# Performance work log

Measured on AMD Instinct MI355X. Metric: run time of the kernel, lower is better.

Reference implementation:

```python
import jax, jax.numpy as jnp
import numpy as np

B, S, D = 8, 4096, 2048
E, TOP_K = 64, 2


def setup_inputs() -> dict:
    key = jax.random.key(0)
    kx, kw, kb = jax.random.split(key, 3)
    x = jax.random.normal(kx, (B, S, D), dtype=jnp.float32)
    # nn.Linear(input_dim, num_experts): weight [E, D], bias [E]
    bound = 1.0 / np.sqrt(D)
    W = jax.random.uniform(kw, (E, D), dtype=jnp.float32, minval=-bound, maxval=bound)
    b = jax.random.uniform(kb, (E,), dtype=jnp.float32, minval=-bound, maxval=bound)
    return {"x": x, "W": W, "b": b}


def reference(x, W, b):
    # mean-pool over sequence dim (x is 3D -> x.mean(dim=1))
    x_flat = jnp.mean(x, axis=1)                      # [B, D]
    logits = jnp.einsum('bd,ed->be', x_flat, W) + b   # [B, E]
    top_k_logits, top_k_indices = jax.lax.top_k(logits, TOP_K)  # [B, K] each
    weights = jax.nn.softmax(top_k_logits, axis=1)    # [B, K]
    return weights, top_k_indices
```

## Files before the change

### kernel.cpp

```cpp
#include <hip/hip_runtime.h>
#include <hip/hip_bf16.h>
#include <math.h>

#define BB 8
#define SS 4096
#define DD 2048
#define EE 64
#define NCHUNK 64
#define ROWS_PER_CHUNK (SS / NCHUNK)

__global__ void mean_partial_kernel(const float* __restrict__ x,
                                    float* __restrict__ partial) {
    int blk   = blockIdx.x;
    int h     = blk & 1;
    int c     = (blk >> 1) & (NCHUNK - 1);
    int b     = blk >> 7;
    int d     = h * (DD / 2) + threadIdx.x * 4;

    const float4* xp = (const float4*)(x + (size_t)b * SS * DD
                                         + (size_t)c * ROWS_PER_CHUNK * DD
                                         + d);
    float4 a0 = make_float4(0.f, 0.f, 0.f, 0.f);
    float4 a1 = make_float4(0.f, 0.f, 0.f, 0.f);
    float4 a2 = make_float4(0.f, 0.f, 0.f, 0.f);
    float4 a3 = make_float4(0.f, 0.f, 0.f, 0.f);
    const size_t rs = DD / 4;
    #pragma unroll 4
    for (int r = 0; r < ROWS_PER_CHUNK; r += 4) {
        float4 v0 = xp[(size_t)(r + 0) * rs];
        float4 v1 = xp[(size_t)(r + 1) * rs];
        float4 v2 = xp[(size_t)(r + 2) * rs];
        float4 v3 = xp[(size_t)(r + 3) * rs];
        a0.x += v0.x; a0.y += v0.y; a0.z += v0.z; a0.w += v0.w;
        a1.x += v1.x; a1.y += v1.y; a1.z += v1.z; a1.w += v1.w;
        a2.x += v2.x; a2.y += v2.y; a2.z += v2.z; a2.w += v2.w;
        a3.x += v3.x; a3.y += v3.y; a3.z += v3.z; a3.w += v3.w;
    }
    float4 acc;
    acc.x = (a0.x + a1.x) + (a2.x + a3.x);
    acc.y = (a0.y + a1.y) + (a2.y + a3.y);
    acc.z = (a0.z + a1.z) + (a2.z + a3.z);
    acc.w = (a0.w + a1.w) + (a2.w + a3.w);
    float4* pp = (float4*)(partial + ((size_t)c * BB + b) * DD + d);
    *pp = acc;
}

__global__ void gate_kernel(const float* __restrict__ partial,
                            const float* __restrict__ W,
                            const float* __restrict__ bias,
                            float* __restrict__ out) {
    __shared__ float xs[DD];
    __shared__ float lred[4][EE];
    __shared__ float logits[EE];

    int b   = blockIdx.x;
    int tid = threadIdx.x;

    for (int d = tid; d < DD; d += 256) {
        float s = 0.f;
        #pragma unroll 8
        for (int c = 0; c < NCHUNK; ++c)
            s += partial[((size_t)c * BB + b) * DD + d];
        xs[d] = s * (1.0f / SS);
    }
    __syncthreads();

    int e = tid & 63;
    int q = tid >> 6;
    const int QD = DD / 4;
    const float* wp = W + (size_t)e * DD + q * QD;
    const float* xq = xs + q * QD;
    float acc = 0.f;
    #pragma unroll 4
    for (int d = 0; d < QD; ++d) acc += xq[d] * wp[d];
    lred[q][e] = acc;
    __syncthreads();

    if (tid < EE) {
        logits[tid] = lred[0][tid] + lred[1][tid] + lred[2][tid] + lred[3][tid]
                      + bias[tid];
    }
    __syncthreads();

    if (tid == 0) {
        float m1 = -INFINITY, m2 = -INFINITY;
        int i1 = 0, i2 = 0;
        for (int i = 0; i < EE; ++i) {
            float v = logits[i];
            if (v > m1) { m2 = m1; i2 = i1; m1 = v; i1 = i; }
            else if (v > m2) { m2 = v; i2 = i; }
        }
        float e2 = expf(m2 - m1);
        float inv = 1.0f / (1.0f + e2);
        out[b * 2 + 0] = inv;
        out[b * 2 + 1] = e2 * inv;
        out[2 * BB + b * 2 + 0] = (float)i1;
        out[2 * BB + b * 2 + 1] = (float)i2;
    }
}

extern "C" void kernel_launch(void* const* d_in, const int* in_sizes, int n_in,
                              void* d_out, int out_size, void* d_ws, size_t ws_size,
                              hipStream_t stream) {
    const float* x  = (const float*)d_in[0];
    const float* W  = (const float*)d_in[1];
    const float* bb = (const float*)d_in[2];
    float* out      = (float*)d_out;
    float* partial  = (float*)d_ws;

    mean_partial_kernel<<<BB * NCHUNK * 2, 256, 0, stream>>>(x, partial);
    gate_kernel<<<BB, 256, 0, stream>>>(partial, W, bb, out);
}
```

Measured before the change: 401.8 us.

## Fuse gating dot product into streaming mean kernel, emit partial logits

The chunked sequence sum is now dotted with the matching half of W inside the streaming kernel using shared memory. Each block writes 64 partial logits instead of a 1024-float partial sum. The gate kernel then only reduces 128 partial logit vectors per batch, applies the 1/S scale and bias, and does top-2. This removes the slow serial reduction and dot product that ran in just 8 blocks. The cost is repeated W reads across blocks, which are expected to be served from cache, and more work per streaming block.

```diff
diff --git a/kernel.cpp b/kernel.cpp
--- a/kernel.cpp
+++ b/kernel.cpp
@@ -7,26 +7,32 @@
 #define DD 2048
 #define EE 64
 #define NCHUNK 64
-#define ROWS_PER_CHUNK (SS / NCHUNK)
+#define ROWS (SS / NCHUNK)
+#define NSLICE (NCHUNK * 2)
 
-__global__ void mean_partial_kernel(const float* __restrict__ x,
-                                    float* __restrict__ partial) {
-    int blk   = blockIdx.x;
-    int h     = blk & 1;
-    int c     = (blk >> 1) & (NCHUNK - 1);
-    int b     = blk >> 7;
-    int d     = h * (DD / 2) + threadIdx.x * 4;
+__global__ void __launch_bounds__(256, 4)
+fused_stream_kernel(const float* __restrict__ x,
+                    const float* __restrict__ W,
+                    float* __restrict__ plogit) {
+    __shared__ float xs[DD / 2];
+    __shared__ float lred[4][EE];
+
+    int blk = blockIdx.x;
+    int h   = blk & 1;
+    int c   = (blk >> 1) & (NCHUNK - 1);
+    int b   = blk >> 7;
+    int tid = threadIdx.x;
+    int d   = h * (DD / 2) + tid * 4;
 
     const float4* xp = (const float4*)(x + (size_t)b * SS * DD
-                                         + (size_t)c * ROWS_PER_CHUNK * DD
-                                         + d);
+                                         + (size_t)c * ROWS * DD + d);
     float4 a0 = make_float4(0.f, 0.f, 0.f, 0.f);
     float4 a1 = make_float4(0.f, 0.f, 0.f, 0.f);
     float4 a2 = make_float4(0.f, 0.f, 0.f, 0.f);
     float4 a3 = make_float4(0.f, 0.f, 0.f, 0.f);
     const size_t rs = DD / 4;
     #pragma unroll 4
-    for (int r = 0; r < ROWS_PER_CHUNK; r += 4) {
+    for (int r = 0; r < ROWS; r += 4) {
         float4 v0 = xp[(size_t)(r + 0) * rs];
         float4 v1 = xp[(size_t)(r + 1) * rs];
         float4 v2 = xp[(size_t)(r + 2) * rs];
@@ -41,44 +47,52 @@
     acc.y = (a0.y + a1.y) + (a2.y + a3.y);
     acc.z = (a0.z + a1.z) + (a2.z + a3.z);
     acc.w = (a0.w + a1.w) + (a2.w + a3.w);
-    float4* pp = (float4*)(partial + ((size_t)c * BB + b) * DD + d);
-    *pp = acc;
+    ((float4*)xs)[tid] = acc;
+    __syncthreads();
+
+    int e = tid & 63;
+    int q = tid >> 6;
+    const int QF4 = (DD / 2 / 4) / 4;
+    const float4* wp = (const float4*)(W + (size_t)e * DD
+                                         + h * (DD / 2) + q * (QF4 * 4));
+    const float4* xq = (const float4*)(xs + q * (QF4 * 4));
+    float dot = 0.f;
+    #pragma unroll 8
+    for (int i = 0; i < QF4; ++i) {
+        float4 wv = wp[i];
+        float4 xv = xq[i];
+        dot += wv.x * xv.x + wv.y * xv.y + wv.z * xv.z + wv.w * xv.w;
+    }
+    lred[q][e] = dot;
+    __syncthreads();
+
+    if (tid < EE) {
+        plogit[(size_t)blk * EE + tid] =
+            lred[0][tid] + lred[1][tid] + lred[2][tid] + lred[3][tid];
+    }
 }
 
-__global__ void gate_kernel(const float* __restrict__ partial,
-                            const float* __restrict__ W,
+__global__ void gate_kernel(const float* __restrict__ plogit,
                             const float* __restrict__ bias,
                             float* __restrict__ out) {
-    __shared__ float xs[DD];
     __shared__ float lred[4][EE];
     __shared__ float logits[EE];
 
     int b   = blockIdx.x;
     int tid = threadIdx.x;
+    int e   = tid & 63;
+    int g   = tid >> 6;
 
-    for (int d = tid; d < DD; d += 256) {
-        float s = 0.f;
-        #pragma unroll 8
-        for (int c = 0; c < NCHUNK; ++c)
-            s += partial[((size_t)c * BB + b) * DD + d];
-        xs[d] = s * (1.0f / SS);
-    }
-    __syncthreads();
-
-    int e = tid & 63;
-    int q = tid >> 6;
-    const int QD = DD / 4;
-    const float* wp = W + (size_t)e * DD + q * QD;
-    const float* xq = xs + q * QD;
-    float acc = 0.f;
-    #pragma unroll 4
-    for (int d = 0; d < QD; ++d) acc += xq[d] * wp[d];
-    lred[q][e] = acc;
+    float s = 0.f;
+    #pragma unroll 8
+    for (int j = g * (NSLICE / 4); j < (g + 1) * (NSLICE / 4); ++j)
+        s += plogit[((size_t)b * NSLICE + j) * EE + e];
+    lred[g][e] = s;
     __syncthreads();
 
     if (tid < EE) {
-        logits[tid] = lred[0][tid] + lred[1][tid] + lred[2][tid] + lred[3][tid]
-                      + bias[tid];
+        logits[tid] = (lred[0][tid] + lred[1][tid] + lred[2][tid] + lred[3][tid])
+                      * (1.0f / SS) + bias[tid];
     }
     __syncthreads();
 
@@ -106,8 +120,8 @@
     const float* W  = (const float*)d_in[1];
     const float* bb = (const float*)d_in[2];
     float* out      = (float*)d_out;
-    float* partial  = (float*)d_ws;
+    float* plogit   = (float*)d_ws;
 
-    mean_partial_kernel<<<BB * NCHUNK * 2, 256, 0, stream>>>(x, partial);
-    gate_kernel<<<BB, 256, 0, stream>>>(partial, W, bb, out);
+    fused_stream_kernel<<<BB * NCHUNK * 2, 256, 0, stream>>>(x, W, plogit);
+    gate_kernel<<<BB, 256, 0, stream>>>(plogit, bb, out);
 }
```

Result: faster. 376.9 us (-6.2%).
